# Kernel tuning notes

Hardware: AMD Instinct MI355X
Metric: run time of the kernel (lower is better)

Reference implementation:

```python
import jax, jax.numpy as jnp
import numpy as np

N_NODES = 100000
N_EDGES = 1600000
D_IN, D_HID, D_OUT = 128, 256, 128


def setup_inputs() -> dict:
    key = jax.random.key(0)
    ks = jax.random.split(key, 9)
    s = lambda d: 1.0 / np.sqrt(d)
    x = jax.random.normal(ks[0], (N_NODES, D_IN), dtype=jnp.float32)
    edge_index = jax.random.randint(ks[1], (2, N_EDGES), 0, N_NODES, dtype=jnp.int64)
    return {
        "x": x,
        "edge_index": edge_index,
        "Wl1": jax.random.normal(ks[2], (D_IN, D_HID), jnp.float32) * s(D_IN),
        "Wr1": jax.random.normal(ks[3], (D_IN, D_HID), jnp.float32) * s(D_IN),
        "b1": jnp.zeros((D_HID,), jnp.float32),
        "Wl2": jax.random.normal(ks[4], (D_HID, D_HID), jnp.float32) * s(D_HID),
        "Wr2": jax.random.normal(ks[5], (D_HID, D_HID), jnp.float32) * s(D_HID),
        "b2": jnp.zeros((D_HID,), jnp.float32),
        "Wl3": jax.random.normal(ks[6], (D_HID, D_OUT), jnp.float32) * s(D_HID),
        "Wr3": jax.random.normal(ks[7], (D_HID, D_OUT), jnp.float32) * s(D_HID),
        "b3": jnp.zeros((D_OUT,), jnp.float32),
    }


def _sage_conv(x, src, dst, Wl, Wr, b):
    # PyG SAGEConv (mean aggr): out = lin_l(mean_{j in N(i)} x_j) + lin_r(x_i)
    msg = x[src]                                                  # [E, d] gather
    agg = jax.ops.segment_sum(msg, dst, num_segments=N_NODES)    # [N, d] scatter-add
    cnt = jax.ops.segment_sum(jnp.ones((src.shape[0],), x.dtype), dst,
                              num_segments=N_NODES)
    mean = agg / jnp.maximum(cnt, 1.0)[:, None]
    return mean @ Wl + x @ Wr + b


def reference(x, edge_index, Wl1, Wr1, b1, Wl2, Wr2, b2, Wl3, Wr3, b3):
    src, dst = edge_index[0], edge_index[1]
    h = jax.nn.relu(_sage_conv(x, src, dst, Wl1, Wr1, b1))
    h = jax.nn.relu(_sage_conv(h, src, dst, Wl2, Wr2, b2))
    h = jax.nn.relu(_sage_conv(h, src, dst, Wl3, Wr3, b3))
    return h
```

## Files before the change

kernel.cpp:

```cpp
#include <hip/hip_runtime.h>
#include <hip/hip_bf16.h>

#define N_NODES 100000
#define NBUK 391
#define CHUNK 4096

typedef unsigned short ushort_t;
typedef unsigned char uchar_t;
typedef __attribute__((ext_vector_type(8))) short bf16x8;
typedef __attribute__((ext_vector_type(4))) float f32x4;
typedef __attribute__((ext_vector_type(2))) float f32x2;

__device__ inline float bfbits2f(unsigned int lo16) { return __uint_as_float(lo16 << 16); }

__device__ inline ushort_t f2bfbits(float f) {
    __hip_bfloat16 h = __float2bfloat16(f);
    return *reinterpret_cast<ushort_t*>(&h);
}

__device__ inline unsigned int pk2bf(float lo, float hi) {
    return (unsigned int)f2bfbits(lo) | ((unsigned int)f2bfbits(hi) << 16);
}

__device__ inline uchar_t f2fp8(float f) {
    int p = __builtin_amdgcn_cvt_pk_fp8_f32(f, 0.0f, 0, false);
    return (uchar_t)(p & 0xff);
}

__device__ inline void acc8_fp8(float* a, unsigned int ux, unsigned int uy) {
    f32x2 f01 = __builtin_amdgcn_cvt_pk_f32_fp8(ux, false);
    f32x2 f23 = __builtin_amdgcn_cvt_pk_f32_fp8(ux, true);
    f32x2 f45 = __builtin_amdgcn_cvt_pk_f32_fp8(uy, false);
    f32x2 f67 = __builtin_amdgcn_cvt_pk_f32_fp8(uy, true);
    a[0] += f01.x; a[1] += f01.y; a[2] += f23.x; a[3] += f23.y;
    a[4] += f45.x; a[5] += f45.y; a[6] += f67.x; a[7] += f67.y;
}

__device__ inline void acc16_fp8(float* a, uint4 u) {
    acc8_fp8(a, u.x, u.y);
    acc8_fp8(a + 8, u.z, u.w);
}

__global__ __launch_bounds__(256) void scan1(const int* __restrict__ in, int* __restrict__ out,
                                             int* __restrict__ bsum, int n) {
    __shared__ int lds[256];
    const int t = threadIdx.x;
    const int base = blockIdx.x * 1024 + t * 4;
    int4 v = {0, 0, 0, 0};
    if (base + 3 < n) v = *(const int4*)(in + base);
    else {
        v.x = (base + 0 < n) ? in[base + 0] : 0;
        v.y = (base + 1 < n) ? in[base + 1] : 0;
        v.z = (base + 2 < n) ? in[base + 2] : 0;
        v.w = (base + 3 < n) ? in[base + 3] : 0;
    }
    int s0 = v.x, s1 = s0 + v.y, s2 = s1 + v.z, s3 = s2 + v.w;
    lds[t] = s3;
    __syncthreads();
    for (int off = 1; off < 256; off <<= 1) {
        int a = (t >= off) ? lds[t - off] : 0;
        __syncthreads();
        lds[t] += a;
        __syncthreads();
    }
    const int texcl = lds[t] - s3;
    if (t == 255) bsum[blockIdx.x] = lds[255];
    if (base + 0 < n) out[base + 0] = texcl;
    if (base + 1 < n) out[base + 1] = texcl + s0;
    if (base + 2 < n) out[base + 2] = texcl + s1;
    if (base + 3 < n) out[base + 3] = texcl + s2;
}

__global__ __launch_bounds__(256) void scan2(int* __restrict__ bsum, int nb) {
    __shared__ int lds[256];
    const int t = threadIdx.x;
    int v = (t < nb) ? bsum[t] : 0;
    lds[t] = v;
    __syncthreads();
    for (int off = 1; off < 256; off <<= 1) {
        int a = (t >= off) ? lds[t - off] : 0;
        __syncthreads();
        lds[t] += a;
        __syncthreads();
    }
    if (t < nb) bsum[t] = lds[t] - v;
}

__global__ void scan3(int* __restrict__ out, const int* __restrict__ bsum, int n, int E) {
    int i = blockIdx.x * blockDim.x + threadIdx.x;
    if (i < n) out[i] += bsum[i >> 10];
    if (i == 0) out[n] = E;
}

__global__ __launch_bounds__(256) void hist1(const int* __restrict__ dst, int* __restrict__ H,
                                             int E, int NC) {
    __shared__ int h[NBUK + 1];
    const int t = threadIdx.x, c = blockIdx.x;
    for (int g = t; g <= NBUK; g += 256) h[g] = 0;
    __syncthreads();
    const long base = (long)c * CHUNK;
#pragma unroll 4
    for (int it = 0; it < CHUNK / 256; ++it) {
        long e = base + it * 256 + t;
        if (e < E) atomicAdd(&h[((unsigned)dst[e]) >> 8], 1);
    }
    __syncthreads();
    for (int g = t; g < NBUK; g += 256) H[(size_t)g * NC + c] = h[g];
}

__global__ __launch_bounds__(256) void binA(const int* __restrict__ src,
                                            const int* __restrict__ dst,
                                            const int* __restrict__ Hs,
                                            uint2* __restrict__ tmp, int E, int NC) {
    __shared__ int cur[NBUK + 1];
    const int t = threadIdx.x, c = blockIdx.x;
    for (int g = t; g < NBUK; g += 256) cur[g] = Hs[(size_t)g * NC + c];
    __syncthreads();
    const long cb = (long)c * CHUNK;
#pragma unroll 4
    for (int it = 0; it < CHUNK / 256; ++it) {
        long e = cb + it * 256 + t;
        if (e < E) {
            unsigned d = (unsigned)dst[e];
            int pos = atomicAdd(&cur[d >> 8], 1);
            uint2 p = {d, (unsigned)src[e]};
            tmp[pos] = p;
        }
    }
}

__global__ __launch_bounds__(256) void hist2_inv(const uint2* __restrict__ tmp,
                                                 const int* __restrict__ Hs,
                                                 int* __restrict__ cnt,
                                                 float* __restrict__ invd, int NC) {
    __shared__ int h[256];
    const int t = threadIdx.x, b = blockIdx.x;
    h[t] = 0;
    __syncthreads();
    const int beg = Hs[(size_t)b * NC], end = Hs[(size_t)(b + 1) * NC];
    for (int e = beg + t; e < end; e += 256) atomicAdd(&h[tmp[e].x & 255u], 1);
    __syncthreads();
    const int d = b * 256 + t;
    if (d < N_NODES) {
        cnt[d] = h[t];
        invd[d] = 1.0f / (float)max(h[t], 1);
    }
}

__global__ __launch_bounds__(256) void scatter2(const uint2* __restrict__ tmp,
                                                const int* __restrict__ Hs,
                                                const int* __restrict__ roff,
                                                int* __restrict__ csr, int NC) {
    __shared__ int cur[256];
    const int t = threadIdx.x, b = blockIdx.x;
    const int d = b * 256 + t;
    cur[t] = (d <= N_NODES) ? roff[min(d, N_NODES)] : 0;
    __syncthreads();
    const int beg = Hs[(size_t)b * NC], end = Hs[(size_t)(b + 1) * NC];
    for (int e = beg + t; e < end; e += 256) {
        uint2 p = tmp[e];
        int pos = atomicAdd(&cur[p.x & 255u], 1);
        csr[pos] = (int)p.y;
    }
}

__global__ void round_both(const float* __restrict__ x, ushort_t* __restrict__ xb,
                           uchar_t* __restrict__ x8, long n) {
    long i = ((long)blockIdx.x * blockDim.x + threadIdx.x) * 4;
    if (i < n) {
        float4 v = *(const float4*)(x + i);
        ushort4 o = {f2bfbits(v.x), f2bfbits(v.y), f2bfbits(v.z), f2bfbits(v.w)};
        *(ushort4*)(xb + i) = o;
        int w = __builtin_amdgcn_cvt_pk_fp8_f32(v.x, v.y, 0, false);
        w = __builtin_amdgcn_cvt_pk_fp8_f32(v.z, v.w, w, true);
        *(unsigned int*)(x8 + i) = (unsigned int)w;
    }
}

__global__ void cvt_transpose(const float* __restrict__ W, ushort_t* __restrict__ WT,
                              int K, int J, int kdst0, int ldwt) {
    int idx = blockIdx.x * blockDim.x + threadIdx.x;
    if (idx >= K * J) return;
    int k = idx / J, j = idx - k * J;
    WT[(size_t)j * ldwt + kdst0 + k] = f2bfbits(W[idx]);
}

__global__ void cvt6(const float* __restrict__ Wl2, const float* __restrict__ Wr2,
                     const float* __restrict__ Wl3, const float* __restrict__ Wr3,
                     ushort_t* __restrict__ WT2A, ushort_t* __restrict__ WT2B,
                     ushort_t* __restrict__ WT3) {
    const int y = blockIdx.y;
    int idx = blockIdx.x * blockDim.x + threadIdx.x;
    if (idx >= 256 * 128) return;
    int k = idx >> 7, jj = idx & 127;
    const float* W;
    ushort_t* WT;
    int J = 256, jsrc0 = 0;
    switch (y) {
        case 0: W = Wl2; WT = WT2A; break;
        case 1: W = Wr2; WT = WT2A; break;
        case 2: W = Wl2; WT = WT2B; jsrc0 = 128; break;
        case 3: W = Wr2; WT = WT2B; jsrc0 = 128; break;
        case 4: W = Wl3; WT = WT3; J = 128; break;
        default: W = Wr3; WT = WT3; J = 128; break;
    }
    const int row0 = (y & 1) * 128;
    WT[(size_t)(row0 + jj) * 256 + k] = f2bfbits(W[(size_t)k * J + jsrc0 + jj]);
}

template <bool ADDZ, typename OT>
__global__ __launch_bounds__(256) void gather_mean(const uchar_t* __restrict__ Y,
                                                   const ushort_t* __restrict__ Z,
                                                   const int* __restrict__ roff,
                                                   const int* __restrict__ csr,
                                                   const float* __restrict__ invd,
                                                   OT* __restrict__ out, int out_ld, int col0) {
    const int w = (blockIdx.x * blockDim.x + threadIdx.x) >> 6;
    if (w >= N_NODES) return;
    const int lane = threadIdx.x & 63;
    const int g = lane >> 4;
    const int l = lane & 15;
    const int e0 = roff[w], e1 = roff[w + 1];

    float a[8] = {0.f, 0.f, 0.f, 0.f, 0.f, 0.f, 0.f, 0.f};

    int e = e0 + g;
    for (; e + 12 < e1; e += 16) {
        const int s0 = csr[e], s1 = csr[e + 4], s2 = csr[e + 8], s3 = csr[e + 12];
        uint2 u0 = *(const uint2*)(Y + (size_t)s0 * 128 + l * 8);
        uint2 u1 = *(const uint2*)(Y + (size_t)s1 * 128 + l * 8);
        uint2 u2 = *(const uint2*)(Y + (size_t)s2 * 128 + l * 8);
        uint2 u3 = *(const uint2*)(Y + (size_t)s3 * 128 + l * 8);
        acc8_fp8(a, u0.x, u0.y); acc8_fp8(a, u1.x, u1.y);
        acc8_fp8(a, u2.x, u2.y); acc8_fp8(a, u3.x, u3.y);
    }
    for (; e < e1; e += 4) {
        uint2 u0 = *(const uint2*)(Y + (size_t)csr[e] * 128 + l * 8);
        acc8_fp8(a, u0.x, u0.y);
    }

#pragma unroll
    for (int i = 0; i < 8; ++i) {
        a[i] += __shfl_xor(a[i], 16);
        a[i] += __shfl_xor(a[i], 32);
    }

    if (g != 0) return;
    const float iv = invd[w];
#pragma unroll
    for (int i = 0; i < 8; ++i) a[i] *= iv;

    if constexpr (ADDZ) {
        uint4 z = *(const uint4*)(Z + (size_t)w * 128 + l * 8);
        float zf[8];
        zf[0] = bfbits2f(z.x & 0xffffu); zf[1] = __uint_as_float(z.x & 0xffff0000u);
        zf[2] = bfbits2f(z.y & 0xffffu); zf[3] = __uint_as_float(z.y & 0xffff0000u);
        zf[4] = bfbits2f(z.z & 0xffffu); zf[5] = __uint_as_float(z.z & 0xffff0000u);
        zf[6] = bfbits2f(z.w & 0xffffu); zf[7] = __uint_as_float(z.w & 0xffff0000u);
#pragma unroll
        for (int i = 0; i < 8; ++i) a[i] = fmaxf(a[i] + zf[i], 0.0f);
    }

    if constexpr (sizeof(OT) == 4) {
        float* op = (float*)out + (size_t)w * out_ld + col0 + l * 8;
        float4 s0 = {a[0], a[1], a[2], a[3]};
        float4 s1 = {a[4], a[5], a[6], a[7]};
        *(float4*)op = s0;
        *(float4*)(op + 4) = s1;
    } else {
        ushort_t* op = (ushort_t*)out + (size_t)w * out_ld + col0 + l * 8;
        ushort4 lohi0 = {f2bfbits(a[0]), f2bfbits(a[1]), f2bfbits(a[2]), f2bfbits(a[3])};
        ushort4 lohi1 = {f2bfbits(a[4]), f2bfbits(a[5]), f2bfbits(a[6]), f2bfbits(a[7])};
        *(ushort4*)op = lohi0;
        *(ushort4*)(op + 4) = lohi1;
    }
}

__global__ __launch_bounds__(256) void gather256(const uchar_t* __restrict__ Y,
                                                 const ushort_t* __restrict__ Z,
                                                 const int* __restrict__ roff,
                                                 const int* __restrict__ csr,
                                                 const float* __restrict__ invd,
                                                 ushort_t* __restrict__ out) {
    const int w = (blockIdx.x * blockDim.x + threadIdx.x) >> 6;
    if (w >= N_NODES) return;
    const int lane = threadIdx.x & 63;
    const int g = lane >> 4;
    const int l = lane & 15;
    const int e0 = roff[w], e1 = roff[w + 1];

    float a[16];
#pragma unroll
    for (int i = 0; i < 16; ++i) a[i] = 0.0f;

    int e = e0 + g;
    for (; e + 12 < e1; e += 16) {
        const int s0 = csr[e], s1 = csr[e + 4], s2 = csr[e + 8], s3 = csr[e + 12];
        uint4 u0 = *(const uint4*)(Y + (size_t)s0 * 256 + l * 16);
        uint4 u1 = *(const uint4*)(Y + (size_t)s1 * 256 + l * 16);
        uint4 u2 = *(const uint4*)(Y + (size_t)s2 * 256 + l * 16);
        uint4 u3 = *(const uint4*)(Y + (size_t)s3 * 256 + l * 16);
        acc16_fp8(a, u0); acc16_fp8(a, u1); acc16_fp8(a, u2); acc16_fp8(a, u3);
    }
    for (; e < e1; e += 4) {
        uint4 u0 = *(const uint4*)(Y + (size_t)csr[e] * 256 + l * 16);
        acc16_fp8(a, u0);
    }

#pragma unroll
    for (int i = 0; i < 16; ++i) {
        a[i] += __shfl_xor(a[i], 16);
        a[i] += __shfl_xor(a[i], 32);
    }

    if (g != 0) return;
    const float iv = invd[w];

    uint4 z0 = *(const uint4*)(Z + (size_t)w * 256 + l * 16);
    uint4 z1 = *(const uint4*)(Z + (size_t)w * 256 + l * 16 + 8);
    float zf[16];
    zf[0] = bfbits2f(z0.x & 0xffffu);  zf[1] = __uint_as_float(z0.x & 0xffff0000u);
    zf[2] = bfbits2f(z0.y & 0xffffu);  zf[3] = __uint_as_float(z0.y & 0xffff0000u);
    zf[4] = bfbits2f(z0.z & 0xffffu);  zf[5] = __uint_as_float(z0.z & 0xffff0000u);
    zf[6] = bfbits2f(z0.w & 0xffffu);  zf[7] = __uint_as_float(z0.w & 0xffff0000u);
    zf[8] = bfbits2f(z1.x & 0xffffu);  zf[9] = __uint_as_float(z1.x & 0xffff0000u);
    zf[10] = bfbits2f(z1.y & 0xffffu); zf[11] = __uint_as_float(z1.y & 0xffff0000u);
    zf[12] = bfbits2f(z1.z & 0xffffu); zf[13] = __uint_as_float(z1.z & 0xffff0000u);
    zf[14] = bfbits2f(z1.w & 0xffffu); zf[15] = __uint_as_float(z1.w & 0xffff0000u);

#pragma unroll
    for (int i = 0; i < 16; ++i) a[i] = fmaxf(a[i] * iv + zf[i], 0.0f);

    ushort_t* op = out + (size_t)w * 256 + l * 16;
    uint4 s0, s1;
    s0.x = pk2bf(a[0], a[1]);   s0.y = pk2bf(a[2], a[3]);
    s0.z = pk2bf(a[4], a[5]);   s0.w = pk2bf(a[6], a[7]);
    s1.x = pk2bf(a[8], a[9]);   s1.y = pk2bf(a[10], a[11]);
    s1.z = pk2bf(a[12], a[13]); s1.w = pk2bf(a[14], a[15]);
    *(uint4*)op = s0;
    *(uint4*)(op + 8) = s1;
}

template <int KH, bool CONCAT, int MODE>
__global__ __launch_bounds__(256) void mfma_gemm256(const ushort_t* __restrict__ A,
                                                    const ushort_t* __restrict__ A2,
                                                    const ushort_t* __restrict__ WT,
                                                    const float* __restrict__ bias,
                                                    void* __restrict__ out0p, int ld0,
                                                    ushort_t* __restrict__ out1, int ld1) {
    constexpr int KTOT = CONCAT ? 2 * KH : KH;
    constexpr int BK = 64;
    __shared__ ushort_t smem[24576];
    ushort_t* As = smem;
    ushort_t* Bs = smem + 8192;

    const int tid = threadIdx.x;
    const int lane = tid & 63;
    const int w = tid >> 6;
    const int wr = w >> 1, wc = w & 1;
    const int n0 = blockIdx.x * 128;

    const int srow = lane >> 3;
    const int skc = (lane & 7) ^ srow;

    f32x4 acc0[4][4], acc1[4][4];
#pragma unroll
    for (int m = 0; m < 4; ++m)
#pragma unroll
        for (int n = 0; n < 4; ++n) {
            acc0[m][n] = (f32x4){0.f, 0.f, 0.f, 0.f};
            acc1[m][n] = (f32x4){0.f, 0.f, 0.f, 0.f};
        }

    for (int k0 = 0; k0 < KTOT; k0 += BK) {
        const ushort_t* Asrc = A;
        int ak = k0;
        if (CONCAT && k0 >= KH) { Asrc = A2; ak = k0 - KH; }
#pragma unroll
        for (int i = 0; i < 4; ++i) {
            const int ci = w * 4 + i;
            int grow = n0 + ci * 8 + srow;
            grow = min(grow, N_NODES - 1);
            const ushort_t* g = Asrc + (size_t)grow * KH + ak + skc * 8;
            __builtin_amdgcn_global_load_lds((const unsigned int*)g,
                                             (unsigned int*)(As + ci * 512), 16, 0, 0);
        }
#pragma unroll
        for (int i = 0; i < 8; ++i) {
            const int ci = w * 8 + i;
            const int jrow = ci * 8 + srow;
            const ushort_t* g = WT + (size_t)jrow * KTOT + k0 + skc * 8;
            __builtin_amdgcn_global_load_lds((const unsigned int*)g,
                                             (unsigned int*)(Bs + ci * 512), 16, 0, 0);
        }
        __syncthreads();

#pragma unroll
        for (int kk = 0; kk < 2; ++kk) {
            const int kc = kk * 4 + (lane >> 4);
            bf16x8 af[4], b0[4], b1[4];
#pragma unroll
            for (int m = 0; m < 4; ++m) {
                const int row = wr * 64 + m * 16 + (lane & 15);
                af[m] = *(const bf16x8*)((const char*)As + row * 128 + ((kc ^ (row & 7)) << 4));
            }
#pragma unroll
            for (int n = 0; n < 4; ++n) {
                const int r0 = wc * 64 + n * 16 + (lane & 15);
                const int r1 = 128 + r0;
                b0[n] = *(const bf16x8*)((const char*)Bs + r0 * 128 + ((kc ^ (r0 & 7)) << 4));
                b1[n] = *(const bf16x8*)((const char*)Bs + r1 * 128 + ((kc ^ (r1 & 7)) << 4));
            }
#pragma unroll
            for (int m = 0; m < 4; ++m)
#pragma unroll
                for (int n = 0; n < 4; ++n) {
                    acc0[m][n] = __builtin_amdgcn_mfma_f32_16x16x32_bf16(af[m], b0[n],
                                                                         acc0[m][n], 0, 0, 0);
                    acc1[m][n] = __builtin_amdgcn_mfma_f32_16x16x32_bf16(af[m], b1[n],
                                                                         acc1[m][n], 0, 0, 0);
                }
        }
        __syncthreads();
    }

    const int c15 = lane & 15;
    const int r4 = (lane >> 4) * 4;
#pragma unroll
    for (int m = 0; m < 4; ++m) {
#pragma unroll
        for (int q = 0; q < 4; ++q) {
            const int row_g = n0 + wr * 64 + m * 16 + r4 + q;
            if (row_g >= N_NODES) continue;
#pragma unroll
            for (int n = 0; n < 4; ++n) {
                const int lcol = wc * 64 + n * 16 + c15;
                const float v0 = acc0[m][n][q];
                const float v1 = acc1[m][n][q];
                if constexpr (MODE == 0) {
                    ushort_t* o = (ushort_t*)out0p;
                    o[(size_t)row_g * ld0 + lcol] = f2bfbits(fmaxf(v0 + bias[lcol], 0.0f));
                    o[(size_t)row_g * ld0 + 128 + lcol] =
                        f2bfbits(fmaxf(v1 + bias[128 + lcol], 0.0f));
                } else {
                    ((uchar_t*)out0p)[(size_t)row_g * ld0 + lcol] = f2fp8(v0);
                    out1[(size_t)row_g * ld1 + lcol] = f2bfbits(v1 + bias[lcol]);
                }
            }
        }
    }
}

extern "C" void kernel_launch(void* const* d_in, const int* in_sizes, int n_in,
                              void* d_out, int out_size, void* d_ws, size_t ws_size,
                              hipStream_t stream) {
    const float* x   = (const float*)d_in[0];
    const int*   ei  = (const int*)d_in[1];
    const float* Wl1 = (const float*)d_in[2];
    const float* Wr1 = (const float*)d_in[3];
    const float* b1  = (const float*)d_in[4];
    const float* Wl2 = (const float*)d_in[5];
    const float* Wr2 = (const float*)d_in[6];
    const float* b2  = (const float*)d_in[7];
    const float* Wl3 = (const float*)d_in[8];
    const float* Wr3 = (const float*)d_in[9];
    const float* b3  = (const float*)d_in[10];

    const int E = in_sizes[1] / 2;
    const int* src = ei;
    const int* dst = ei + E;
    const int N = N_NODES;
    const int NC = (E + CHUNK - 1) / CHUNK;
    const int nH = NBUK * NC;

    char* ws = (char*)d_ws;
    float* invd = (float*)(ws + 0);
    int* cnt    = (int*)(ws + 400000);
    int* roff   = (int*)(ws + 800000);
    int* bsum   = (int*)(ws + 1200016);
    int* H      = (int*)(ws + 1201040);
    ushort_t* WT1  = (ushort_t*)(ws + 1812568);
    ushort_t* WT2A = (ushort_t*)(ws + 1943640);
    ushort_t* WT2B = (ushort_t*)(ws + 2074712);
    ushort_t* WT3  = (ushort_t*)(ws + 2205784);
    uint2* tmp  = (uint2*)(ws + 2336864);
    int* csr    = (int*)(ws + 15136864);
    ushort_t* h1 = (ushort_t*)(ws + 21536864);
    ushort_t* h2 = (ushort_t*)(ws + 72736864);
    ushort_t* M1 = h2;
    ushort_t* T1 = (ushort_t*)(ws + 123936864);
    const size_t WS_NEED = 149536864;
    if (ws_size < WS_NEED) return;

    uchar_t* T8  = (uchar_t*)tmp;
    uchar_t* T1a = (uchar_t*)T1;
    ushort_t* Zd = (ushort_t*)d_out;
    ushort_t* Zh = h1;

    const int GX = (N + 127) / 128;
    const int NBH = (nH + 1023) / 1024;
    const int NBN = (N + 1023) / 1024;

    hist1<<<NC, 256, 0, stream>>>(dst, H, E, NC);
    scan1<<<NBH, 256, 0, stream>>>(H, H, bsum, nH);
    scan2<<<1, 256, 0, stream>>>(bsum, NBH);
    scan3<<<(nH + 256) / 256, 256, 0, stream>>>(H, bsum, nH, E);
    binA<<<NC, 256, 0, stream>>>(src, dst, H, tmp, E, NC);
    hist2_inv<<<NBUK, 256, 0, stream>>>(tmp, H, cnt, invd, NC);
    scan1<<<NBN, 256, 0, stream>>>(cnt, roff, bsum, N);
    scan2<<<1, 256, 0, stream>>>(bsum, NBN);
    scan3<<<(N + 256) / 256, 256, 0, stream>>>(roff, bsum, N, E);
    scatter2<<<NBUK, 256, 0, stream>>>(tmp, H, roff, csr, NC);

    cvt_transpose<<<(128 * 256 + 255) / 256, 256, 0, stream>>>(Wl1, WT1, 128, 256, 0, 256);
    cvt_transpose<<<(128 * 256 + 255) / 256, 256, 0, stream>>>(Wr1, WT1, 128, 256, 128, 256);
    cvt6<<<dim3(128, 6), 256, 0, stream>>>(Wl2, Wr2, Wl3, Wr3, WT2A, WT2B, WT3);

    round_both<<<(N * 128 / 4 + 255) / 256, 256, 0, stream>>>(x, T1, T8, (long)N * 128);
    gather_mean<false, ushort_t><<<(N * 64 + 255) / 256, 256, 0, stream>>>(
        T8, nullptr, roff, csr, invd, M1, 128, 0);
    mfma_gemm256<128, true, 0><<<GX, 256, 0, stream>>>(
        M1, T1, WT1, b1, h1, 256, nullptr, 0);

    mfma_gemm256<256, false, 1><<<GX, 256, 0, stream>>>(
        h1, nullptr, WT2A, b2 + 0, T1a, 256, Zd, 256);
    mfma_gemm256<256, false, 1><<<GX, 256, 0, stream>>>(
        h1, nullptr, WT2B, b2 + 128, T1a + 128, 256, Zd + 128, 256);
    gather256<<<(N * 64 + 255) / 256, 256, 0, stream>>>(
        T1a, Zd, roff, csr, invd, h2);

    mfma_gemm256<256, false, 1><<<GX, 256, 0, stream>>>(
        h2, nullptr, WT3, b3, T8, 128, Zh, 128);
    gather_mean<true, float><<<(N * 64 + 255) / 256, 256, 0, stream>>>(
        T8, Zh, roff, csr, invd, (float*)d_out, 128, 0);
}
```

Baseline: 506.9 us.

## Double-buffer LDS tiles in MFMA GEMM with smaller K step

Halves the K tile from 64 to 32 and splits shared memory into two buffers, so the next tile's global-to-LDS loads are issued while MFMAs run on the current tile. The swizzle pattern is adjusted to the 64-byte row width. This is meant to hide global load latency behind compute and to drop one barrier per iteration. The cost is twice as many iterations and barriers per K, a fully unrolled loop that adds code size, and a swizzle that may cause more LDS bank conflicts with the narrower rows.

```diff
diff --git a/kernel.cpp b/kernel.cpp
--- a/kernel.cpp
+++ b/kernel.cpp
@@ -349,10 +349,9 @@
                                                     void* __restrict__ out0p, int ld0,
                                                     ushort_t* __restrict__ out1, int ld1) {
     constexpr int KTOT = CONCAT ? 2 * KH : KH;
-    constexpr int BK = 64;
-    __shared__ ushort_t smem[24576];
-    ushort_t* As = smem;
-    ushort_t* Bs = smem + 8192;
+    constexpr int BK = 32;
+    constexpr int NT = KTOT / BK;
+    __shared__ ushort_t smem[2][12288];
 
     const int tid = threadIdx.x;
     const int lane = tid & 63;
@@ -360,8 +359,8 @@
     const int wr = w >> 1, wc = w & 1;
     const int n0 = blockIdx.x * 128;
 
-    const int srow = lane >> 3;
-    const int skc = (lane & 7) ^ srow;
+    const int srow = lane >> 2;
+    const int skc = (lane & 3) ^ ((srow >> 1) & 3);
 
     f32x4 acc0[4][4], acc1[4][4];
 #pragma unroll
@@ -372,57 +371,70 @@
             acc1[m][n] = (f32x4){0.f, 0.f, 0.f, 0.f};
         }
 
-    for (int k0 = 0; k0 < KTOT; k0 += BK) {
+    auto STAGE = [&](int b, int t) {
+        const int k0 = t * BK;
         const ushort_t* Asrc = A;
         int ak = k0;
         if (CONCAT && k0 >= KH) { Asrc = A2; ak = k0 - KH; }
 #pragma unroll
-        for (int i = 0; i < 4; ++i) {
-            const int ci = w * 4 + i;
-            int grow = n0 + ci * 8 + srow;
+        for (int i = 0; i < 2; ++i) {
+            const int ci = w * 2 + i;
+            int grow = n0 + ci * 16 + srow;
             grow = min(grow, N_NODES - 1);
             const ushort_t* g = Asrc + (size_t)grow * KH + ak + skc * 8;
             __builtin_amdgcn_global_load_lds((const unsigned int*)g,
-                                             (unsigned int*)(As + ci * 512), 16, 0, 0);
-        }
-#pragma unroll
-        for (int i = 0; i < 8; ++i) {
-            const int ci = w * 8 + i;
-            const int jrow = ci * 8 + srow;
+                                             (unsigned int*)(&smem[b][ci * 512]), 16, 0, 0);
+        }
+#pragma unroll
+        for (int i = 0; i < 4; ++i) {
+            const int ci = w * 4 + i;
+            const int jrow = ci * 16 + srow;
             const ushort_t* g = WT + (size_t)jrow * KTOT + k0 + skc * 8;
             __builtin_amdgcn_global_load_lds((const unsigned int*)g,
-                                             (unsigned int*)(Bs + ci * 512), 16, 0, 0);
-        }
+                                             (unsigned int*)(&smem[b][4096 + ci * 512]), 16, 0, 0);
+        }
+    };
+
+    auto COMPUTE = [&](int b) {
+        const int kc = lane >> 4;
+        bf16x8 af[4], b0[4], b1[4];
+#pragma unroll
+        for (int m = 0; m < 4; ++m) {
+            const int row = wr * 64 + m * 16 + (lane & 15);
+            const int slot = kc ^ ((row >> 1) & 3);
+            af[m] = *(const bf16x8*)((const char*)&smem[b][0] + row * 64 + slot * 16);
+        }
+#pragma unroll
+        for (int n = 0; n < 4; ++n) {
+            const int r0 = wc * 64 + n * 16 + (lane & 15);
+            const int r1 = 128 + r0;
+            const int s0 = kc ^ ((r0 >> 1) & 3);
+            const int s1 = kc ^ ((r1 >> 1) & 3);
+            b0[n] = *(const bf16x8*)((const char*)&smem[b][4096] + r0 * 64 + s0 * 16);
+            b1[n] = *(const bf16x8*)((const char*)&smem[b][4096] + r1 * 64 + s1 * 16);
+        }
+#pragma unroll
+        for (int m = 0; m < 4; ++m)
+#pragma unroll
+            for (int n = 0; n < 4; ++n) {
+                acc0[m][n] = __builtin_amdgcn_mfma_f32_16x16x32_bf16(af[m], b0[n],
+                                                                     acc0[m][n], 0, 0, 0);
+                acc1[m][n] = __builtin_amdgcn_mfma_f32_16x16x32_bf16(af[m], b1[n],
+                                                                     acc1[m][n], 0, 0, 0);
+            }
+    };
+
+    STAGE(0, 0);
+    __syncthreads();
+    int cur = 0;
+#pragma unroll
+    for (int t = 0; t < NT - 1; ++t) {
+        STAGE(cur ^ 1, t + 1);
+        COMPUTE(cur);
         __syncthreads();
-
-#pragma unroll
-        for (int kk = 0; kk < 2; ++kk) {
-            const int kc = kk * 4 + (lane >> 4);
-            bf16x8 af[4], b0[4], b1[4];
-#pragma unroll
-            for (int m = 0; m < 4; ++m) {
-                const int row = wr * 64 + m * 16 + (lane & 15);
-                af[m] = *(const bf16x8*)((const char*)As + row * 128 + ((kc ^ (row & 7)) << 4));
-            }
-#pragma unroll
-            for (int n = 0; n < 4; ++n) {
-                const int r0 = wc * 64 + n * 16 + (lane & 15);
-                const int r1 = 128 + r0;
-                b0[n] = *(const bf16x8*)((const char*)Bs + r0 * 128 + ((kc ^ (r0 & 7)) << 4));
-                b1[n] = *(const bf16x8*)((const char*)Bs + r1 * 128 + ((kc ^ (r1 & 7)) << 4));
-            }
-#pragma unroll
-            for (int m = 0; m < 4; ++m)
-#pragma unroll
-                for (int n = 0; n < 4; ++n) {
-                    acc0[m][n] = __builtin_amdgcn_mfma_f32_16x16x32_bf16(af[m], b0[n],
-                                                                         acc0[m][n], 0, 0, 0);
-                    acc1[m][n] = __builtin_amdgcn_mfma_f32_16x16x32_bf16(af[m], b1[n],
-                                                                         acc1[m][n], 0, 0, 0);
-                }
-        }
-        __syncthreads();
-    }
+        cur ^= 1;
+    }
+    COMPUTE(cur);
 
     const int c15 = lane & 15;
     const int r4 = (lane >> 4) * 4;
```

Result: faster. 447.4 us, median of 2 (-11.7%).
